# Performance work log

Hardware: AMD Instinct MI355X
Metric: run time of the kernel (lower is better)

The kernel has to match this reference:

```python
import jax, jax.numpy as jnp
import numpy as np

B, C_IN, H, W_IN = 32, 128, 64, 64
C_OUT, K = 256, 3


def setup_inputs() -> dict:
    key = jax.random.key(0)
    kx, kw = jax.random.split(key)
    x = jax.random.normal(kx, (B, C_IN, H, W_IN), dtype=jnp.float32)
    # original initializes weights as binary {0,1} floats
    W = jax.random.randint(kw, (C_OUT, C_IN, K, K), 0, 2).astype(jnp.float32)
    return {"x": x, "W": W}


def reference(x, W):
    # XOR-style conv: out[b,co,ho,wo] = sum(patch * (1 - 2*W[co]))
    # stride=1, padding=0 (hardcoded in the original forward).
    eff_w = 1.0 - 2.0 * W  # (C_OUT, C_IN, K, K)
    return jax.lax.conv_general_dilated(
        x, eff_w,
        window_strides=(1, 1),
        padding='VALID',
        dimension_numbers=('NCHW', 'OIHW', 'NCHW'),
    )
```

## Files before the change

### kernel.cpp

```cpp
#include <hip/hip_runtime.h>


typedef __bf16 bf16x8 __attribute__((ext_vector_type(8)));
typedef float  f32x4  __attribute__((ext_vector_type(4)));

__global__ void prepack_w_kernel(const float* __restrict__ Wf,
                                 unsigned short* __restrict__ effw) {
  int idx = blockIdx.x * 256 + threadIdx.x;
  if (idx >= 36 * 16 * 64 * 8) return;
  int j    = idx & 7;
  int lane = (idx >> 3) & 63;
  int tile = (idx >> 9) & 15;
  int g    = idx >> 13;
  int e    = g % 9;
  int cc   = g / 9;
  int co = tile * 16 + (lane & 15);
  int ci = cc * 32 + (lane >> 4) * 8 + j;
  float w = Wf[(co * 128 + ci) * 9 + e];
  __bf16 h = (__bf16)(1.0f - 2.0f * w);
  unsigned short u; __builtin_memcpy(&u, &h, 2);
  effw[idx] = u;
}

__global__ void prepack_x_kernel(const float* __restrict__ x,
                                 unsigned short* __restrict__ xp) {
  int idx = blockIdx.x * 256 + threadIdx.x;
  int qp = idx & 3;
  int w  = (idx >> 2) & 63;
  int h  = (idx >> 8) & 63;
  int cc = (idx >> 14) & 3;
  int b  = idx >> 16;
  int q  = qp ^ (w & 3);
  const float* xb = x + (((size_t)(b * 128 + cc * 32 + q * 8)) * 64 + h) * 64 + w;
  unsigned short o[8];
  #pragma unroll
  for (int k = 0; k < 8; ++k) {
    float f = xb[(size_t)k * 4096];
    __bf16 hh = (__bf16)f;
    unsigned short u; __builtin_memcpy(&u, &hh, 2);
    o[k] = u;
  }
  unsigned int w0 = (unsigned)o[0] | ((unsigned)o[1] << 16);
  unsigned int w1 = (unsigned)o[2] | ((unsigned)o[3] << 16);
  unsigned int w2 = (unsigned)o[4] | ((unsigned)o[5] << 16);
  unsigned int w3 = (unsigned)o[6] | ((unsigned)o[7] << 16);
  uint4 v = {w0, w1, w2, w3};
  *(uint4*)(xp + (size_t)idx * 8) = v;
}

__global__ __launch_bounds__(256, 2)
void xorconv_mfma_kernel(const unsigned short* __restrict__ xp,
                         const unsigned short* __restrict__ effw,
                         float* __restrict__ out) {
  __shared__ __align__(16) unsigned short xs[10 * 66 * 32];

  const int tid = threadIdx.x;

  const int lin  = blockIdx.x + 4 * blockIdx.y + 32 * blockIdx.z;
  const int work = (lin & 7) * 128 + (lin >> 3);
  const int bxc   = work & 3;
  const int hbt   = (work >> 2) & 7;
  const int bb    = work >> 5;
  const int co_blk = bxc * 64;
  const int hbase  = hbt * 8;

  const int wv   = tid >> 6;
  const int lane = tid & 63;
  const int quad = lane >> 4;
  const int l16  = lane & 15;

  f32x4 acc[2][4][4];
  #pragma unroll
  for (int rw = 0; rw < 2; ++rw)
    #pragma unroll
    for (int i = 0; i < 4; ++i)
      #pragma unroll
      for (int j = 0; j < 4; ++j)
        acc[rw][i][j] = (f32x4){0.f, 0.f, 0.f, 0.f};

  const unsigned short* wbase = effw + ((size_t)(bxc * 4) * 64 + lane) * 8;
  bf16x8 afb[2][4];
  #pragma unroll
  for (int mt = 0; mt < 4; ++mt)
    afb[0][mt] = *(const bf16x8*)(wbase + mt * 512);

  for (int cc = 0; cc < 4; ++cc) {
    const unsigned short* xpcc = xp + ((size_t)(bb * 4 + cc) * 64) * 2048;
    #pragma unroll
    for (int r = 0; r < 10; ++r) {
      int h_in = hbase + r; if (h_in > 63) h_in = 63;
      *(uint4*)&xs[r * 2112 + tid * 8] =
          *(const uint4*)(xpcc + (size_t)h_in * 2048 + tid * 8);
    }
    __syncthreads();

    #pragma unroll
    for (int e = 0; e < 9; ++e) {
      const int cur = e & 1, nxt = cur ^ 1;
      const int kh = e / 3, kw = e % 3;

      {
        int lin2  = cc * 9 + e;
        int linn  = lin2 < 35 ? lin2 + 1 : 35;
        const unsigned short* wp = wbase + (size_t)linn * 8192;
        #pragma unroll
        for (int mt = 0; mt < 4; ++mt)
          afb[nxt][mt] = *(const bf16x8*)(wp + mt * 512);
      }

      #pragma unroll
      for (int rw = 0; rw < 2; ++rw) {
        const int rr = wv * 2 + rw + kh;
        bf16x8 bfr[4];
        #pragma unroll
        for (int j = 0; j < 4; ++j) {
          int ccol = j * 16 + l16 + kw;
          int slot = quad ^ (ccol & 3);
          bfr[j] = *(const bf16x8*)&xs[rr * 2112 + ccol * 32 + slot * 8];
        }
        #pragma unroll
        for (int mt = 0; mt < 4; ++mt)
          #pragma unroll
          for (int j = 0; j < 4; ++j)
            acc[rw][mt][j] = __builtin_amdgcn_mfma_f32_16x16x32_bf16(
                afb[cur][mt], bfr[j], acc[rw][mt][j], 0, 0, 0);
      }
    }
    __syncthreads();

    #pragma unroll
    for (int mt = 0; mt < 4; ++mt) afb[0][mt] = afb[1][mt];
  }

  #pragma unroll
  for (int rw = 0; rw < 2; ++rw) {
    const int ho = hbase + wv * 2 + rw;
    if (ho < 62) {
      #pragma unroll
      for (int mt = 0; mt < 4; ++mt) {
        const int co = co_blk + mt * 16 + quad * 4;
        #pragma unroll
        for (int j = 0; j < 4; ++j) {
          const int wo = j * 16 + l16;
          if (wo < 62) {
            float* op = out + (((size_t)(bb * 256 + co) * 62 + ho) * 62 + wo);
            #pragma unroll
            for (int rg = 0; rg < 4; ++rg)
              op[(size_t)rg * 3844] = acc[rw][mt][j][rg];
          }
        }
      }
    }
  }
}

extern "C" void kernel_launch(void* const* d_in, const int* in_sizes, int n_in,
                              void* d_out, int out_size, void* d_ws, size_t ws_size,
                              hipStream_t stream) {
  const float* x  = (const float*)d_in[0];
  const float* Wf = (const float*)d_in[1];
  float* out = (float*)d_out;
  unsigned short* xp   = (unsigned short*)d_ws;
  unsigned short* effw = xp + (size_t)16777216;

  prepack_x_kernel<<<dim3(8192), dim3(256), 0, stream>>>(x, xp);
  prepack_w_kernel<<<dim3((36 * 16 * 64 * 8 + 255) / 256), dim3(256), 0, stream>>>(Wf, effw);

  dim3 grid(4, 8, 32);
  xorconv_mfma_kernel<<<grid, dim3(256), 0, stream>>>(xp, effw, out);
}
```

Measured before the change: 242.4 us.

## Double-buffer input rows via global_load_lds, halve row tile, fuse prepack kernels

Each block now covers 4 output rows instead of 8, so there are twice as many blocks and half the accumulators, and launch bounds rise to 3 blocks per SM. Input row slabs for the next channel chunk are loaded straight into a second LDS buffer with global_load_lds while the current chunk is computed. Weight fragments are prefetched two steps ahead in a triple buffer. The two prepack kernels are merged into one launch. The trade-off is that halo rows are reloaded more often (6 rows per 4 outputs rather than 10 per 8), and only one sync separates the buffer swaps, which could race if the async LDS loads are not waited on.

```diff
diff --git a/kernel.cpp b/kernel.cpp
--- a/kernel.cpp
+++ b/kernel.cpp
@@ -4,150 +4,156 @@
 typedef __bf16 bf16x8 __attribute__((ext_vector_type(8)));
 typedef float  f32x4  __attribute__((ext_vector_type(4)));
 
-__global__ void prepack_w_kernel(const float* __restrict__ Wf,
-                                 unsigned short* __restrict__ effw) {
-  int idx = blockIdx.x * 256 + threadIdx.x;
-  if (idx >= 36 * 16 * 64 * 8) return;
-  int j    = idx & 7;
-  int lane = (idx >> 3) & 63;
-  int tile = (idx >> 9) & 15;
-  int g    = idx >> 13;
-  int e    = g % 9;
-  int cc   = g / 9;
-  int co = tile * 16 + (lane & 15);
-  int ci = cc * 32 + (lane >> 4) * 8 + j;
-  float w = Wf[(co * 128 + ci) * 9 + e];
-  __bf16 h = (__bf16)(1.0f - 2.0f * w);
-  unsigned short u; __builtin_memcpy(&u, &h, 2);
-  effw[idx] = u;
+#define GLOADLDS16(gp, lp)                                                    \
+  __builtin_amdgcn_global_load_lds(                                           \
+      (const __attribute__((address_space(1))) unsigned int*)(gp),            \
+      (__attribute__((address_space(3))) unsigned int*)(lp), 16, 0, 0)
+
+__global__ void prepack_kernel(const float* __restrict__ x,
+                               const float* __restrict__ Wf,
+                               unsigned short* __restrict__ xp,
+                               unsigned short* __restrict__ effw) {
+  if (blockIdx.x < 8192) {
+    int idx = blockIdx.x * 256 + threadIdx.x;
+    int qp = idx & 3;
+    int w  = (idx >> 2) & 63;
+    int h  = (idx >> 8) & 63;
+    int cc = (idx >> 14) & 3;
+    int b  = idx >> 16;
+    int q  = qp ^ (w & 3);
+    const float* xb = x + (((size_t)(b * 128 + cc * 32 + q * 8)) * 64 + h) * 64 + w;
+    unsigned short o[8];
+    #pragma unroll
+    for (int k = 0; k < 8; ++k) {
+      float f = xb[(size_t)k * 4096];
+      __bf16 hh = (__bf16)f;
+      unsigned short u; __builtin_memcpy(&u, &hh, 2);
+      o[k] = u;
+    }
+    uint4 v = {(unsigned)o[0] | ((unsigned)o[1] << 16),
+               (unsigned)o[2] | ((unsigned)o[3] << 16),
+               (unsigned)o[4] | ((unsigned)o[5] << 16),
+               (unsigned)o[6] | ((unsigned)o[7] << 16)};
+    *(uint4*)(xp + (size_t)idx * 8) = v;
+  } else {
+    int idx = (blockIdx.x - 8192) * 256 + threadIdx.x;
+    int j    = idx & 7;
+    int lane = (idx >> 3) & 63;
+    int tile = (idx >> 9) & 15;
+    int g    = idx >> 13;
+    int e    = g % 9;
+    int cc   = g / 9;
+    int co = tile * 16 + (lane & 15);
+    int ci = cc * 32 + (lane >> 4) * 8 + j;
+    float w = Wf[(co * 128 + ci) * 9 + e];
+    __bf16 h = (__bf16)(1.0f - 2.0f * w);
+    unsigned short u; __builtin_memcpy(&u, &h, 2);
+    effw[idx] = u;
+  }
 }
 
-__global__ void prepack_x_kernel(const float* __restrict__ x,
-                                 unsigned short* __restrict__ xp) {
-  int idx = blockIdx.x * 256 + threadIdx.x;
-  int qp = idx & 3;
-  int w  = (idx >> 2) & 63;
-  int h  = (idx >> 8) & 63;
-  int cc = (idx >> 14) & 3;
-  int b  = idx >> 16;
-  int q  = qp ^ (w & 3);
-  const float* xb = x + (((size_t)(b * 128 + cc * 32 + q * 8)) * 64 + h) * 64 + w;
-  unsigned short o[8];
-  #pragma unroll
-  for (int k = 0; k < 8; ++k) {
-    float f = xb[(size_t)k * 4096];
-    __bf16 hh = (__bf16)f;
-    unsigned short u; __builtin_memcpy(&u, &hh, 2);
-    o[k] = u;
-  }
-  unsigned int w0 = (unsigned)o[0] | ((unsigned)o[1] << 16);
-  unsigned int w1 = (unsigned)o[2] | ((unsigned)o[3] << 16);
-  unsigned int w2 = (unsigned)o[4] | ((unsigned)o[5] << 16);
-  unsigned int w3 = (unsigned)o[6] | ((unsigned)o[7] << 16);
-  uint4 v = {w0, w1, w2, w3};
-  *(uint4*)(xp + (size_t)idx * 8) = v;
-}
-
-__global__ __launch_bounds__(256, 2)
+__global__ __launch_bounds__(256, 3)
 void xorconv_mfma_kernel(const unsigned short* __restrict__ xp,
                          const unsigned short* __restrict__ effw,
                          float* __restrict__ out) {
-  __shared__ __align__(16) unsigned short xs[10 * 66 * 32];
+  __shared__ __align__(16) unsigned short xs[2][6 * 66 * 32];
 
   const int tid = threadIdx.x;
 
-  const int lin  = blockIdx.x + 4 * blockIdx.y + 32 * blockIdx.z;
-  const int work = (lin & 7) * 128 + (lin >> 3);
+  const int lin  = blockIdx.x;
+  const int work = (lin & 7) * 256 + (lin >> 3);
   const int bxc   = work & 3;
-  const int hbt   = (work >> 2) & 7;
-  const int bb    = work >> 5;
+  const int hbt   = (work >> 2) & 15;
+  const int bb    = work >> 6;
   const int co_blk = bxc * 64;
-  const int hbase  = hbt * 8;
+  const int hbase  = hbt * 4;
 
   const int wv   = tid >> 6;
   const int lane = tid & 63;
   const int quad = lane >> 4;
   const int l16  = lane & 15;
 
-  f32x4 acc[2][4][4];
+  f32x4 acc[4][4];
   #pragma unroll
-  for (int rw = 0; rw < 2; ++rw)
+  for (int i = 0; i < 4; ++i)
     #pragma unroll
-    for (int i = 0; i < 4; ++i)
-      #pragma unroll
-      for (int j = 0; j < 4; ++j)
-        acc[rw][i][j] = (f32x4){0.f, 0.f, 0.f, 0.f};
+    for (int j = 0; j < 4; ++j)
+      acc[i][j] = (f32x4){0.f, 0.f, 0.f, 0.f};
 
   const unsigned short* wbase = effw + ((size_t)(bxc * 4) * 64 + lane) * 8;
-  bf16x8 afb[2][4];
+  bf16x8 afb[3][4];
   #pragma unroll
-  for (int mt = 0; mt < 4; ++mt)
-    afb[0][mt] = *(const bf16x8*)(wbase + mt * 512);
+  for (int g = 0; g < 2; ++g)
+    #pragma unroll
+    for (int mt = 0; mt < 4; ++mt)
+      afb[g][mt] = *(const bf16x8*)(wbase + (size_t)g * 8192 + mt * 512);
 
+  const unsigned short* xpb = xp + (size_t)(bb * 4) * 64 * 2048;
+
+  #pragma unroll
+  for (int k = 0; k < 6; ++k) {
+    int h_in = hbase + k; if (h_in > 63) h_in = 63;
+    GLOADLDS16(xpb + (size_t)h_in * 2048 + tid * 8,
+               &xs[0][k * 2112 + tid * 8]);
+  }
+  __syncthreads();
+
+  #pragma unroll
   for (int cc = 0; cc < 4; ++cc) {
-    const unsigned short* xpcc = xp + ((size_t)(bb * 4 + cc) * 64) * 2048;
+    if (cc < 3) {
+      const unsigned short* s = xpb + (size_t)((cc + 1) * 64) * 2048;
+      #pragma unroll
+      for (int k = 0; k < 6; ++k) {
+        int h_in = hbase + k; if (h_in > 63) h_in = 63;
+        GLOADLDS16(s + (size_t)h_in * 2048 + tid * 8,
+                   &xs[(cc + 1) & 1][k * 2112 + tid * 8]);
+      }
+    }
+
+    const unsigned short* xb = xs[cc & 1];
     #pragma unroll
-    for (int r = 0; r < 10; ++r) {
-      int h_in = hbase + r; if (h_in > 63) h_in = 63;
-      *(uint4*)&xs[r * 2112 + tid * 8] =
-          *(const uint4*)(xpcc + (size_t)h_in * 2048 + tid * 8);
+    for (int e = 0; e < 9; ++e) {
+      const int g  = cc * 9 + e;
+      const int kh = e / 3, kw = e % 3;
+
+      if (g + 2 <= 35) {
+        const unsigned short* wp = wbase + (size_t)(g + 2) * 8192;
+        #pragma unroll
+        for (int mt = 0; mt < 4; ++mt)
+          afb[(g + 2) % 3][mt] = *(const bf16x8*)(wp + mt * 512);
+      }
+
+      const int rr = wv + kh;
+      bf16x8 bfr[4];
+      #pragma unroll
+      for (int j = 0; j < 4; ++j) {
+        int ccol = j * 16 + l16 + kw;
+        int slot = quad ^ (ccol & 3);
+        bfr[j] = *(const bf16x8*)&xb[rr * 2112 + ccol * 32 + slot * 8];
+      }
+      #pragma unroll
+      for (int mt = 0; mt < 4; ++mt)
+        #pragma unroll
+        for (int j = 0; j < 4; ++j)
+          acc[mt][j] = __builtin_amdgcn_mfma_f32_16x16x32_bf16(
+              afb[g % 3][mt], bfr[j], acc[mt][j], 0, 0, 0);
     }
     __syncthreads();
-
-    #pragma unroll
-    for (int e = 0; e < 9; ++e) {
-      const int cur = e & 1, nxt = cur ^ 1;
-      const int kh = e / 3, kw = e % 3;
-
-      {
-        int lin2  = cc * 9 + e;
-        int linn  = lin2 < 35 ? lin2 + 1 : 35;
-        const unsigned short* wp = wbase + (size_t)linn * 8192;
-        #pragma unroll
-        for (int mt = 0; mt < 4; ++mt)
-          afb[nxt][mt] = *(const bf16x8*)(wp + mt * 512);
-      }
-
-      #pragma unroll
-      for (int rw = 0; rw < 2; ++rw) {
-        const int rr = wv * 2 + rw + kh;
-        bf16x8 bfr[4];
-        #pragma unroll
-        for (int j = 0; j < 4; ++j) {
-          int ccol = j * 16 + l16 + kw;
-          int slot = quad ^ (ccol & 3);
-          bfr[j] = *(const bf16x8*)&xs[rr * 2112 + ccol * 32 + slot * 8];
-        }
-        #pragma unroll
-        for (int mt = 0; mt < 4; ++mt)
-          #pragma unroll
-          for (int j = 0; j < 4; ++j)
-            acc[rw][mt][j] = __builtin_amdgcn_mfma_f32_16x16x32_bf16(
-                afb[cur][mt], bfr[j], acc[rw][mt][j], 0, 0, 0);
-      }
-    }
-    __syncthreads();
-
-    #pragma unroll
-    for (int mt = 0; mt < 4; ++mt) afb[0][mt] = afb[1][mt];
   }
 
-  #pragma unroll
-  for (int rw = 0; rw < 2; ++rw) {
-    const int ho = hbase + wv * 2 + rw;
-    if (ho < 62) {
+  const int ho = hbase + wv;
+  if (ho < 62) {
+    #pragma unroll
+    for (int mt = 0; mt < 4; ++mt) {
+      const int co = co_blk + mt * 16 + quad * 4;
       #pragma unroll
-      for (int mt = 0; mt < 4; ++mt) {
-        const int co = co_blk + mt * 16 + quad * 4;
-        #pragma unroll
-        for (int j = 0; j < 4; ++j) {
-          const int wo = j * 16 + l16;
-          if (wo < 62) {
-            float* op = out + (((size_t)(bb * 256 + co) * 62 + ho) * 62 + wo);
-            #pragma unroll
-            for (int rg = 0; rg < 4; ++rg)
-              op[(size_t)rg * 3844] = acc[rw][mt][j][rg];
-          }
+      for (int j = 0; j < 4; ++j) {
+        const int wo = j * 16 + l16;
+        if (wo < 62) {
+          float* op = out + (((size_t)(bb * 256 + co) * 62 + ho) * 62 + wo);
+          #pragma unroll
+          for (int rg = 0; rg < 4; ++rg)
+            op[(size_t)rg * 3844] = acc[mt][j][rg];
         }
       }
     }
@@ -163,9 +169,8 @@
   unsigned short* xp   = (unsigned short*)d_ws;
   unsigned short* effw = xp + (size_t)16777216;
 
-  prepack_x_kernel<<<dim3(8192), dim3(256), 0, stream>>>(x, xp);
-  prepack_w_kernel<<<dim3((36 * 16 * 64 * 8 + 255) / 256), dim3(256), 0, stream>>>(Wf, effw);
+  prepack_kernel<<<dim3(8192 + 1152), dim3(256), 0, stream>>>(x, Wf, xp, effw);
 
-  dim3 grid(4, 8, 32);
+  dim3 grid(2048);
   xorconv_mfma_kernel<<<grid, dim3(256), 0, stream>>>(xp, effw, out);
 }
```

Result: faster. 237.0 us (-2.3%).
